# Optimization experiments

Hardware: AMD Instinct MI355X
Metric: run time of the kernel (lower is better)

## Reference

```python
import jax, jax.numpy as jnp
import numpy as np

EPS = 1e-5


def _whiten(feature):
    # ZCA whitening per sample (WCT): f_w = U diag(s^-1/2) U^T (f - mean)
    b, c, h, w = feature.shape
    f = feature.reshape(b, c, h * w)
    mean = f.mean(axis=-1, keepdims=True)
    f = f - mean
    cov = jnp.einsum('bcx,bdx->bcd', f, f) / (h * w - 1)
    s, u = jnp.linalg.eigh(cov)
    s = jnp.maximum(s, EPS)
    out = jnp.einsum('bcd,bd,bed,bex->bcx', u, s ** -0.5, u, f)
    return out.reshape(b, c, h, w)


def _color(feature, target):
    # ZCA coloring: f_c = Ut diag(st^1/2) Ut^T (f - mean_f) + mean_t
    b, c, h, w = feature.shape
    f = feature.reshape(b, c, h * w)
    f = f - f.mean(axis=-1, keepdims=True)
    t = target.reshape(b, c, -1)
    tmean = t.mean(axis=-1, keepdims=True)
    tc = t - tmean
    cov = jnp.einsum('bcx,bdx->bcd', tc, tc) / (tc.shape[-1] - 1)
    s, u = jnp.linalg.eigh(cov)
    s = jnp.maximum(s, EPS)
    out = jnp.einsum('bcd,bd,bed,bex->bcx', u, s ** 0.5, u, f) + tmean
    return out.reshape(b, c, h, w)


def _patches(f, p):
    # [b,c,h,w] -> [b,c,h,w,p*p], same ordering as torch unfold(2,p).unfold(3,p)
    pad = (p - 1) // 2
    b, c, h, w = f.shape
    fp = jnp.pad(f, ((0, 0), (0, 0), (pad, pad), (pad, pad)))
    return jnp.stack([fp[:, :, i:i + h, j:j + w] for i in range(p) for j in range(p)], axis=-1)


def reference(content_feature, style_feature, style_strength, patch_size):
    p = int(patch_size)
    pad = (p - 1) // 2
    nc = _whiten(content_feature)
    ns = _whiten(style_feature)
    b, c, h, w = nc.shape
    n = h * w  # one style kernel per style spatial location (stride 1)

    # style kernels [b, n, c, p, p] and their L2 norms over (c,p,p)
    sk = _patches(ns, p).transpose(0, 2, 3, 1, 4).reshape(b, n, c, p, p)
    knorm = jnp.sqrt(jnp.sum(sk ** 2, axis=(2, 3, 4), keepdims=True))
    skn = (sk / knorm).reshape(b, n, c, p * p)

    # patch matching score == conv2d of content with normalized style kernels
    cp = _patches(nc, p)                              # [b,c,h,w,p*p]
    score = jnp.einsum('bchwk,bnck->bnhw', cp, skn)   # [b,n,h,w]

    # argmax one-hot -> gather the best-matching (un-normalized) style patch
    idx = jnp.argmax(score, axis=1)                   # [b,h,w]
    sel = jax.vmap(lambda k, i: k[i])(sk, idx.reshape(b, -1))  # [b,hw,c,p,p]
    sel = sel.reshape(b, h, w, c, p, p).transpose(0, 3, 1, 2, 4, 5)  # [b,c,h,w,p,p]

    # overlap-add == conv_transpose2d(one_hot, kernels, padding=p-1) on padded input
    buf = jnp.zeros((b, c, h + p - 1, w + p - 1), dtype=sel.dtype)
    for di in range(p):
        for dj in range(p):
            buf = buf.at[:, :, di:di + h, dj:dj + w].add(sel[:, :, :, :, di, dj])
    recon = buf[:, :, pad:pad + h, pad:pad + w]

    # overlap counts (norm_deconvolution)
    m = jnp.zeros((h + p - 1, w + p - 1), dtype=sel.dtype)
    for di in range(p):
        for dj in range(p):
            m = m.at[di:di + h, dj:dj + w].add(1.0)
    norm = m[pad:pad + h, pad:pad + w]

    reassembled = recon / norm[None, None]
    stylized = _color(reassembled, style_feature)
    return (1.0 - style_strength) * content_feature + style_strength * stylized


def setup_inputs():
    key = jax.random.key(0)
    k1, k2 = jax.random.split(key)
    B, C, H, W = 2, 256, 48, 48
    return {
        'content_feature': jax.random.normal(k1, (B, C, H, W), jnp.float32),
        'style_feature': jax.random.normal(k2, (B, C, H, W), jnp.float32),
        'style_strength': jnp.float32(1.0),
        'patch_size': 3,
    }
```

## Files before the change

### kernel.cpp

```cpp
#include <hip/hip_runtime.h>

constexpr int B_  = 2;
constexpr int C_  = 256;
constexpr int H_  = 48;
constexpr int W_  = 48;
constexpr int N_  = H_ * W_;
constexpr int PH_ = H_ + 2;
constexpr int PW_ = W_ + 2;
constexpr int NP_ = PH_ * PW_;
constexpr int NPS_ = 2560;
constexpr int MS_  = 2560;
constexpr int CC_ = C_ * C_;
constexpr int NCH_ = 36;
constexpr int NC_  = N_ / NCH_;
constexpr int NSIT_ = 5;
constexpr int KCH_ = 9;

__device__ inline float waveRed(float v) {
  #pragma unroll
  for (int o = 32; o > 0; o >>= 1) v += __shfl_down(v, o);
  return v;
}

#define GEMM64_COMPUTE(sAT, sB, acc, ty, tx)                        \
  _Pragma("unroll")                                                 \
  for (int kk = 0; kk < 16; kk++) {                                 \
    float4 a = *(const float4*)&sAT[kk][(ty) * 4];                  \
    float4 b = *(const float4*)&sB[kk][(tx) * 4];                   \
    acc[0][0] += a.x * b.x; acc[0][1] += a.x * b.y;                 \
    acc[0][2] += a.x * b.z; acc[0][3] += a.x * b.w;                 \
    acc[1][0] += a.y * b.x; acc[1][1] += a.y * b.y;                 \
    acc[1][2] += a.y * b.z; acc[1][3] += a.y * b.w;                 \
    acc[2][0] += a.z * b.x; acc[2][1] += a.z * b.y;                 \
    acc[2][2] += a.z * b.z; acc[2][3] += a.z * b.w;                 \
    acc[3][0] += a.w * b.x; acc[3][1] += a.w * b.y;                 \
    acc[3][2] += a.w * b.z; acc[3][3] += a.w * b.w;                 \
  }


__global__ __launch_bounds__(256) void center_kernel(
    const float* __restrict__ content, const float* __restrict__ style,
    float* __restrict__ fc, float* __restrict__ fs, float* __restrict__ mean_s) {
  int t = blockIdx.x;
  int which = t / (B_ * C_);
  int bc = t % (B_ * C_);
  const float* src = which ? style : content;
  float* dst = which ? fs : fc;
  const float* row = src + (size_t)bc * N_;
  float acc = 0.f;
  for (int i = threadIdx.x; i < N_; i += 256) acc += row[i];
  __shared__ float sm[4];
  float r = waveRed(acc);
  if ((threadIdx.x & 63) == 0) sm[threadIdx.x >> 6] = r;
  __syncthreads();
  float mean = (sm[0] + sm[1] + sm[2] + sm[3]) * (1.0f / N_);
  for (int i = threadIdx.x; i < N_; i += 256) dst[(size_t)bc * N_ + i] = row[i] - mean;
  if (which == 1 && threadIdx.x == 0) mean_s[bc] = mean;
}

__global__ __launch_bounds__(256) void cov_kernel(
    const float* __restrict__ fc, const float* __restrict__ fs, float* __restrict__ pcov) {
  int z = blockIdx.z;
  int m = z & 3, ci = z >> 2;
  const float* f = (m < 2) ? (fc + (size_t)m * C_ * N_) : (fs + (size_t)(m - 2) * C_ * N_);
  int i0 = blockIdx.y * 64, j0 = blockIdx.x * 64;
  int t = threadIdx.x;
  int tx = t & 15, ty = t >> 4;
  int sr = t >> 2, skq = t & 3;
  __shared__ float sAT[16][68], sB[16][68];
  float acc[4][4] = {};
  int k0e = ci * 256 + 256;
  for (int k0 = ci * 256; k0 < k0e; k0 += 16) {
    float4 av = *(const float4*)&f[(size_t)(i0 + sr) * N_ + k0 + skq * 4];
    float4 bv = *(const float4*)&f[(size_t)(j0 + sr) * N_ + k0 + skq * 4];
    __syncthreads();
    sAT[skq * 4 + 0][sr] = av.x; sAT[skq * 4 + 1][sr] = av.y;
    sAT[skq * 4 + 2][sr] = av.z; sAT[skq * 4 + 3][sr] = av.w;
    sB[skq * 4 + 0][sr] = bv.x;  sB[skq * 4 + 1][sr] = bv.y;
    sB[skq * 4 + 2][sr] = bv.z;  sB[skq * 4 + 3][sr] = bv.w;
    __syncthreads();
    GEMM64_COMPUTE(sAT, sB, acc, ty, tx)
  }
  float* out = pcov + ((size_t)ci * 4 + m) * CC_;
  for (int u = 0; u < 4; u++)
    for (int v = 0; v < 4; v++)
      out[(size_t)(i0 + ty * 4 + u) * C_ + (j0 + tx * 4 + v)] = acc[u][v];
}

__global__ __launch_bounds__(256) void covreduce(
    const float* __restrict__ pcov, float* __restrict__ A4) {
  int t = blockIdx.x * 256 + threadIdx.x;
  float acc = 0.f;
  #pragma unroll
  for (int ci = 0; ci < KCH_; ci++) acc += pcov[(size_t)ci * 4 * CC_ + t];
  A4[t] = acc * (1.0f / (float)(N_ - 1));
}

__global__ __launch_bounds__(256) void ns_init(
    const float* __restrict__ A4, float* __restrict__ Yp, float* __restrict__ Zp,
    float* __restrict__ scal) {
  int m = blockIdx.y, s = blockIdx.x;
  const float* A = A4 + (size_t)m * CC_;
  float d = A[(size_t)threadIdx.x * 257];
  __shared__ float sm[4];
  float r = waveRed(d);
  if ((threadIdx.x & 63) == 0) sm[threadIdx.x >> 6] = r;
  __syncthreads();
  float trace = sm[0] + sm[1] + sm[2] + sm[3];
  float sc = 1.1f * trace / (float)C_;
  if (s == 0 && threadIdx.x == 0) scal[m] = sc;
  float inv = 1.0f / sc;
  int i0 = s * (CC_ / 16);
  for (int i = i0 + threadIdx.x; i < i0 + CC_ / 16; i += 256) {
    Yp[(size_t)m * CC_ + i] = A[i] * inv;
    Zp[(size_t)m * CC_ + i] = ((i >> 8) == (i & 255)) ? 1.0f : 0.0f;
    Yp[(size_t)(4 + m) * CC_ + i] = 0.f;
    Zp[(size_t)(4 + m) * CC_ + i] = 0.f;
  }
}

__global__ __launch_bounds__(256) void ns_stepA(
    const float* __restrict__ Zp, const float* __restrict__ Yp, float* __restrict__ Tp) {
  int z = blockIdx.z;
  int m = z & 3, kh = z >> 2;
  const float* A0 = Zp + (size_t)m * CC_;
  const float* A1 = Zp + (size_t)(4 + m) * CC_;
  const float* B0 = Yp + (size_t)m * CC_;
  const float* B1 = Yp + (size_t)(4 + m) * CC_;
  float* out = Tp + (size_t)(kh * 4 + m) * CC_;
  int i0 = blockIdx.y * 32, j0 = blockIdx.x * 32;
  int t = threadIdx.x;
  int tx = t & 15, ty = t >> 4;
  int sr = t >> 3, sc4 = t & 7;
  __shared__ float sAT[32][36], sB[32][36];
  float acc[2][2] = {};
  int k0e = kh * 128 + 128;
  for (int k0 = kh * 128; k0 < k0e; k0 += 32) {
    size_t ia = (size_t)(i0 + sr) * 256 + k0 + sc4 * 4;
    size_t ib = (size_t)(k0 + sr) * 256 + j0 + sc4 * 4;
    float4 a0 = *(const float4*)&A0[ia];
    float4 a1 = *(const float4*)&A1[ia];
    float4 b0 = *(const float4*)&B0[ib];
    float4 b1 = *(const float4*)&B1[ib];
    float4 av = {a0.x + a1.x, a0.y + a1.y, a0.z + a1.z, a0.w + a1.w};
    float4 bv = {b0.x + b1.x, b0.y + b1.y, b0.z + b1.z, b0.w + b1.w};
    __syncthreads();
    sAT[sc4 * 4 + 0][sr] = av.x; sAT[sc4 * 4 + 1][sr] = av.y;
    sAT[sc4 * 4 + 2][sr] = av.z; sAT[sc4 * 4 + 3][sr] = av.w;
    *(float4*)&sB[sr][sc4 * 4] = bv;
    __syncthreads();
    #pragma unroll
    for (int kk = 0; kk < 32; kk++) {
      float2 a = *(const float2*)&sAT[kk][ty * 2];
      float2 b = *(const float2*)&sB[kk][tx * 2];
      acc[0][0] += a.x * b.x; acc[0][1] += a.x * b.y;
      acc[1][0] += a.y * b.x; acc[1][1] += a.y * b.y;
    }
    __syncthreads();
  }
  for (int u = 0; u < 2; u++)
    for (int v = 0; v < 2; v++) {
      int i = i0 + ty * 2 + u, j = j0 + tx * 2 + v;
      float d = (kh == 0 && i == j) ? 3.0f : 0.0f;
      out[(size_t)i * 256 + j] = d - acc[u][v];
    }
}

__global__ __launch_bounds__(256) void ns_stepB(
    const float* __restrict__ Yp, const float* __restrict__ Zp, const float* __restrict__ Tp,
    float* __restrict__ Ynp, float* __restrict__ Znp) {
  int z = blockIdx.z;
  int m = z & 3, kh = (z >> 2) & 1;
  bool doY = (z < 8);
  const float* A0 = (doY ? Yp : Tp) + (size_t)m * CC_;
  const float* A1 = (doY ? Yp : Tp) + (size_t)(4 + m) * CC_;
  const float* B0 = (doY ? Tp : Zp) + (size_t)m * CC_;
  const float* B1 = (doY ? Tp : Zp) + (size_t)(4 + m) * CC_;
  float* out = (doY ? Ynp : Znp) + (size_t)(kh * 4 + m) * CC_;
  int i0 = blockIdx.y * 32, j0 = blockIdx.x * 32;
  int t = threadIdx.x;
  int tx = t & 15, ty = t >> 4;
  int sr = t >> 3, sc4 = t & 7;
  __shared__ float sAT[32][36], sB[32][36];
  float acc[2][2] = {};
  int k0e = kh * 128 + 128;
  for (int k0 = kh * 128; k0 < k0e; k0 += 32) {
    size_t ia = (size_t)(i0 + sr) * 256 + k0 + sc4 * 4;
    size_t ib = (size_t)(k0 + sr) * 256 + j0 + sc4 * 4;
    float4 a0 = *(const float4*)&A0[ia];
    float4 a1 = *(const float4*)&A1[ia];
    float4 b0 = *(const float4*)&B0[ib];
    float4 b1 = *(const float4*)&B1[ib];
    float4 av = {a0.x + a1.x, a0.y + a1.y, a0.z + a1.z, a0.w + a1.w};
    float4 bv = {b0.x + b1.x, b0.y + b1.y, b0.z + b1.z, b0.w + b1.w};
    __syncthreads();
    sAT[sc4 * 4 + 0][sr] = av.x; sAT[sc4 * 4 + 1][sr] = av.y;
    sAT[sc4 * 4 + 2][sr] = av.z; sAT[sc4 * 4 + 3][sr] = av.w;
    *(float4*)&sB[sr][sc4 * 4] = bv;
    __syncthreads();
    #pragma unroll
    for (int kk = 0; kk < 32; kk++) {
      float2 a = *(const float2*)&sAT[kk][ty * 2];
      float2 b = *(const float2*)&sB[kk][tx * 2];
      acc[0][0] += a.x * b.x; acc[0][1] += a.x * b.y;
      acc[1][0] += a.y * b.x; acc[1][1] += a.y * b.y;
    }
    __syncthreads();
  }
  for (int u = 0; u < 2; u++)
    for (int v = 0; v < 2; v++) {
      int i = i0 + ty * 2 + u, j = j0 + tx * 2 + v;
      out[(size_t)i * 256 + j] = 0.5f * acc[u][v];
    }
}

__global__ __launch_bounds__(256) void whiten_pad(
    const float* __restrict__ Zf, const float* __restrict__ scal,
    const float* __restrict__ fc, const float* __restrict__ fs,
    float* __restrict__ ncP, float* __restrict__ nsP, float* __restrict__ nsT) {
  int m = blockIdx.z;
  const float* f = (m < 2) ? (fc + (size_t)m * C_ * N_) : (fs + (size_t)(m - 2) * C_ * N_);
  int c0 = blockIdx.y * 64, x0 = blockIdx.x * 64;
  int t = threadIdx.x;
  int tx = t & 15, ty = t >> 4;
  int sr = t >> 2, skq = t & 3;
  int bkk = t & 15, bc4 = t >> 4;
  __shared__ float sAT[16][68], sB[16][68];
  float acc[4][4] = {};
  for (int k0 = 0; k0 < 256; k0 += 16) {
    size_t ia = (size_t)(c0 + sr) * 256 + k0 + skq * 4;
    float4 a0 = *(const float4*)&Zf[(size_t)m * CC_ + ia];
    float4 a1 = *(const float4*)&Zf[(size_t)(4 + m) * CC_ + ia];
    float4 av = {a0.x + a1.x, a0.y + a1.y, a0.z + a1.z, a0.w + a1.w};
    float4 bv = *(const float4*)&f[(size_t)(k0 + bkk) * N_ + x0 + bc4 * 4];
    __syncthreads();
    sAT[skq * 4 + 0][sr] = av.x; sAT[skq * 4 + 1][sr] = av.y;
    sAT[skq * 4 + 2][sr] = av.z; sAT[skq * 4 + 3][sr] = av.w;
    *(float4*)&sB[bkk][bc4 * 4] = bv;
    __syncthreads();
    GEMM64_COMPUTE(sAT, sB, acc, ty, tx)
  }
  float rs = rsqrtf(scal[m]);
  int b = (m < 2) ? m : (m - 2);
  for (int u = 0; u < 4; u++)
    for (int v = 0; v < 4; v++) {
      int c = c0 + ty * 4 + u, x = x0 + tx * 4 + v;
      int h = x / W_, w = x % W_;
      int pp = (h + 1) * PW_ + (w + 1);
      float val = acc[u][v] * rs;
      if (m < 2) {
        ncP[((size_t)b * C_ + c) * NPS_ + pp] = val;
      } else {
        nsP[((size_t)b * NP_ + pp) * C_ + c] = val;
        nsT[((size_t)b * C_ + c) * NPS_ + pp] = val;
      }
    }
}

__global__ __launch_bounds__(256) void q_kernel(const float* __restrict__ nsP, float* __restrict__ q) {
  int wid = (blockIdx.x * 256 + threadIdx.x) >> 6;
  int lane = threadIdx.x & 63;
  if (wid >= B_ * NP_) return;
  const float* v = nsP + (size_t)wid * C_;
  float acc = 0.f;
  #pragma unroll
  for (int c = lane; c < C_; c += 64) { float t = v[c]; acc += t * t; }
  acc = waveRed(acc);
  if (lane == 0) q[wid] = acc;
}

__global__ __launch_bounds__(256) void kninv_kernel(const float* __restrict__ q, float* __restrict__ kninv) {
  int t = blockIdx.x * 256 + threadIdx.x;
  if (t >= B_ * N_) return;
  int b = t / N_, n = t % N_;
  int hn = n / W_, wn = n % W_;
  const float* qb = q + (size_t)b * NP_ + hn * PW_ + wn;
  float s = 0.f;
  #pragma unroll
  for (int i = 0; i < 3; i++)
    #pragma unroll
    for (int j = 0; j < 3; j++) s += qb[i * PW_ + j];
  kninv[t] = rsqrtf(s);
}

__global__ __launch_bounds__(256) void m_kernel(
    const float* __restrict__ At, const float* __restrict__ Bt, float* __restrict__ M,
    size_t batchA, size_t batchM) {
  size_t bz = blockIdx.z;
  At += bz * batchA; Bt += bz * batchA; M += bz * batchM;
  int i0 = blockIdx.y * 64, j0 = blockIdx.x * 128;
  int t = threadIdx.x;
  int tx = t & 15, ty = t >> 4;
  int akk = t >> 4, ac4 = t & 15;
  int bkk = t >> 5, bc4 = t & 31;
  __shared__ float sA[16][68], sB[16][132];
  float acc[4][8] = {};
  for (int k0 = 0; k0 < 256; k0 += 16) {
    float4 a0 = *(const float4*)&At[(size_t)(k0 + akk) * NPS_ + i0 + ac4 * 4];
    float4 b0 = *(const float4*)&Bt[(size_t)(k0 + bkk) * NPS_ + j0 + bc4 * 4];
    float4 b1 = *(const float4*)&Bt[(size_t)(k0 + bkk + 8) * NPS_ + j0 + bc4 * 4];
    __syncthreads();
    *(float4*)&sA[akk][ac4 * 4] = a0;
    *(float4*)&sB[bkk][bc4 * 4] = b0;
    *(float4*)&sB[bkk + 8][bc4 * 4] = b1;
    __syncthreads();
    #pragma unroll
    for (int kk = 0; kk < 16; kk++) {
      float4 a  = *(const float4*)&sA[kk][ty * 4];
      float4 p  = *(const float4*)&sB[kk][tx * 4];
      float4 qv = *(const float4*)&sB[kk][64 + tx * 4];
      acc[0][0] += a.x * p.x; acc[0][1] += a.x * p.y; acc[0][2] += a.x * p.z; acc[0][3] += a.x * p.w;
      acc[1][0] += a.y * p.x; acc[1][1] += a.y * p.y; acc[1][2] += a.y * p.z; acc[1][3] += a.y * p.w;
      acc[2][0] += a.z * p.x; acc[2][1] += a.z * p.y; acc[2][2] += a.z * p.z; acc[2][3] += a.z * p.w;
      acc[3][0] += a.w * p.x; acc[3][1] += a.w * p.y; acc[3][2] += a.w * p.z; acc[3][3] += a.w * p.w;
      acc[0][4] += a.x * qv.x; acc[0][5] += a.x * qv.y; acc[0][6] += a.x * qv.z; acc[0][7] += a.x * qv.w;
      acc[1][4] += a.y * qv.x; acc[1][5] += a.y * qv.y; acc[1][6] += a.y * qv.z; acc[1][7] += a.y * qv.w;
      acc[2][4] += a.z * qv.x; acc[2][5] += a.z * qv.y; acc[2][6] += a.z * qv.z; acc[2][7] += a.z * qv.w;
      acc[3][4] += a.w * qv.x; acc[3][5] += a.w * qv.y; acc[3][6] += a.w * qv.z; acc[3][7] += a.w * qv.w;
    }
    __syncthreads();
  }
  #pragma unroll
  for (int u = 0; u < 4; u++) {
    size_t row = (size_t)(i0 + ty * 4 + u) * MS_;
    float4 s0 = {acc[u][0], acc[u][1], acc[u][2], acc[u][3]};
    float4 s1 = {acc[u][4], acc[u][5], acc[u][6], acc[u][7]};
    *(float4*)&M[row + j0 + tx * 4] = s0;
    *(float4*)&M[row + j0 + 64 + tx * 4] = s1;
  }
}

__global__ __launch_bounds__(256) void score_kernel(
    const float* __restrict__ M, const float* __restrict__ kninv,
    float* __restrict__ pval, int* __restrict__ pidx, int b0, size_t batchM) {
  int b = b0 + blockIdx.z;
  M += (size_t)blockIdx.z * batchM;
  int m = blockIdx.x * 256 + threadIdx.x;
  int h = m / W_, w = m % W_;
  int cm = h * PW_ + w;
  int n0 = blockIdx.y * NC_;
  const float* kni = kninv + (size_t)b * N_;
  float best = -3.4e38f;
  int bidx = n0;
  for (int n = n0; n < n0 + NC_; n++) {
    int hn = n / W_, wn = n % W_;
    int rn = hn * PW_ + wn;
    const float* base = M + (size_t)rn * MS_ + cm;
    float s = 0.f;
    #pragma unroll
    for (int i = 0; i < 3; i++)
      #pragma unroll
      for (int j = 0; j < 3; j++) s += base[(size_t)(i * PW_ + j) * (MS_ + 1)];
    s *= kni[n];
    if (s > best) { best = s; bidx = n; }
  }
  pval[((size_t)b * NCH_ + blockIdx.y) * N_ + m] = best;
  pidx[((size_t)b * NCH_ + blockIdx.y) * N_ + m] = bidx;
}

__global__ __launch_bounds__(256) void argmax_final(
    const float* __restrict__ pval, const int* __restrict__ pidx, int* __restrict__ idxb) {
  int t = blockIdx.x * 256 + threadIdx.x;
  if (t >= B_ * N_) return;
  int b = t / N_, m = t % N_;
  float best = -3.4e38f; int bidx = 0;
  for (int ch = 0; ch < NCH_; ch++) {
    float v = pval[((size_t)b * NCH_ + ch) * N_ + m];
    int i = pidx[((size_t)b * NCH_ + ch) * N_ + m];
    if (v > best) { best = v; bidx = i; }
  }
  idxb[t] = bidx;
}

__global__ __launch_bounds__(256) void reassemble_kernel(
    const float* __restrict__ nsP, const int* __restrict__ idxb, float* __restrict__ recon) {
  int bm = blockIdx.x;
  int b = bm / N_, m = bm % N_;
  int h = m / W_, w = m % W_;
  int c = threadIdx.x;
  float acc = 0.f; int cnt = 0;
  for (int di = 0; di < 3; di++) {
    int hs = h + 1 - di; if (hs < 0 || hs >= H_) continue;
    for (int dj = 0; dj < 3; dj++) {
      int ws = w + 1 - dj; if (ws < 0 || ws >= W_) continue;
      int n = idxb[(size_t)b * N_ + hs * W_ + ws];
      int hn = n / W_, wn = n % W_;
      int pp = (hn + di) * PW_ + (wn + dj);
      acc += nsP[((size_t)b * NP_ + pp) * C_ + c];
      cnt++;
    }
  }
  recon[((size_t)b * N_ + m) * C_ + c] = acc / (float)cnt;
}

__global__ __launch_bounds__(256) void rmean_part(const float* __restrict__ recon, float* __restrict__ pmr) {
  int b = blockIdx.y, ch = blockIdx.x, c = threadIdx.x;
  float acc = 0.f;
  int x0 = ch * (N_ / 16);
  for (int x = x0; x < x0 + (N_ / 16); x++) acc += recon[((size_t)b * N_ + x) * C_ + c];
  pmr[((size_t)b * 16 + ch) * C_ + c] = acc;
}

__global__ __launch_bounds__(256) void rmean_fin(const float* __restrict__ pmr, float* __restrict__ mr) {
  int b = blockIdx.x, c = threadIdx.x;
  float acc = 0.f;
  for (int ch = 0; ch < 16; ch++) acc += pmr[((size_t)b * 16 + ch) * C_ + c];
  mr[(size_t)b * C_ + c] = acc * (1.0f / N_);
}

__global__ __launch_bounds__(256) void color_blend(
    const float* __restrict__ Yf, const float* __restrict__ scal,
    const float* __restrict__ recon, const float* __restrict__ mr,
    const float* __restrict__ msty, const float* __restrict__ content,
    const float* __restrict__ ssp, float* __restrict__ out) {
  int b = blockIdx.z;
  int m = 2 + b;
  int c0 = blockIdx.y * 64, x0 = blockIdx.x * 64;
  int t = threadIdx.x;
  int tx = t & 15, ty = t >> 4;
  int sr = t >> 2, skq = t & 3;
  __shared__ float sAT[16][68], sB[16][68];
  float acc[4][4] = {};
  for (int k0 = 0; k0 < 256; k0 += 16) {
    size_t ia = (size_t)(c0 + sr) * 256 + k0 + skq * 4;
    float4 a0 = *(const float4*)&Yf[(size_t)m * CC_ + ia];
    float4 a1 = *(const float4*)&Yf[(size_t)(4 + m) * CC_ + ia];
    float4 av = {a0.x + a1.x, a0.y + a1.y, a0.z + a1.z, a0.w + a1.w};
    float4 bm4 = *(const float4*)&mr[(size_t)b * C_ + k0 + skq * 4];
    float4 bv = *(const float4*)&recon[((size_t)b * N_ + x0 + sr) * C_ + k0 + skq * 4];
    bv.x -= bm4.x; bv.y -= bm4.y; bv.z -= bm4.z; bv.w -= bm4.w;
    __syncthreads();
    sAT[skq * 4 + 0][sr] = av.x; sAT[skq * 4 + 1][sr] = av.y;
    sAT[skq * 4 + 2][sr] = av.z; sAT[skq * 4 + 3][sr] = av.w;
    sB[skq * 4 + 0][sr] = bv.x;  sB[skq * 4 + 1][sr] = bv.y;
    sB[skq * 4 + 2][sr] = bv.z;  sB[skq * 4 + 3][sr] = bv.w;
    __syncthreads();
    GEMM64_COMPUTE(sAT, sB, acc, ty, tx)
  }
  float sq = sqrtf(scal[m]);
  float ss = ssp[0];
  for (int u = 0; u < 4; u++)
    for (int v = 0; v < 4; v++) {
      int c = c0 + ty * 4 + u, x = x0 + tx * 4 + v;
      float sty = acc[u][v] * sq + msty[(size_t)b * C_ + c];
      size_t o = ((size_t)b * C_ + c) * N_ + x;
      out[o] = (1.0f - ss) * content[o] + ss * sty;
    }
}

extern "C" void kernel_launch(void* const* d_in, const int* in_sizes, int n_in,
                              void* d_out, int out_size, void* d_ws, size_t ws_size,
                              hipStream_t stream) {
  (void)in_sizes; (void)n_in; (void)out_size;
  const float* content = (const float*)d_in[0];
  const float* style   = (const float*)d_in[1];
  const float* ssp     = (const float*)d_in[2];
  float* out = (float*)d_out;
  float* W = (float*)d_ws;

  size_t off = 0;
  float* fc   = W + off; off += (size_t)B_ * C_ * N_;
  float* fs   = W + off; off += (size_t)B_ * C_ * N_;
  float* nsP  = W + off; off += (size_t)B_ * NP_ * C_;
  float* nsT  = W + off; off += (size_t)B_ * C_ * NPS_;
  float* ncP  = W + off; off += (size_t)B_ * C_ * NPS_;
  float* A4   = W + off; off += (size_t)4 * CC_;
  float* Ya   = W + off; off += (size_t)8 * CC_;
  float* Yb   = W + off; off += (size_t)8 * CC_;
  float* Za   = W + off; off += (size_t)8 * CC_;
  float* Zb   = W + off; off += (size_t)8 * CC_;
  float* scal = W + off; off += 4;
  float* msty = W + off; off += (size_t)B_ * C_;
  float* mr   = W + off; off += (size_t)B_ * C_;
  float* pmr  = W + off; off += (size_t)B_ * 16 * C_;
  float* q    = W + off; off += (size_t)B_ * NP_;
  float* kni  = W + off; off += (size_t)B_ * N_;
  float* pval = W + off; off += (size_t)B_ * NCH_ * N_;
  float* Mb   = W + off;
  size_t off_Mb = off;

  size_t off1 = off_Mb + (size_t)MS_ * MS_;
  size_t off2 = off_Mb + (size_t)2 * MS_ * MS_;
  size_t tail = (size_t)B_ * NCH_ * N_ + (size_t)B_ * N_;
  bool dual = ws_size >= (off2 + tail) * sizeof(float);
  size_t offM = dual ? off2 : off1;
  int* pidx = (int*)(W + offM);
  int* idxb = (int*)(W + offM + (size_t)B_ * NCH_ * N_);
  float* pcov = Mb;
  float* T    = Mb;
  float* recon = fs;

  hipMemsetAsync(nsP, 0, (size_t)B_ * NP_ * C_ * sizeof(float), stream);
  hipMemsetAsync(nsT, 0, (size_t)B_ * C_ * NPS_ * sizeof(float), stream);
  hipMemsetAsync(ncP, 0, (size_t)B_ * C_ * NPS_ * sizeof(float), stream);

  center_kernel<<<2 * B_ * C_, 256, 0, stream>>>(content, style, fc, fs, msty);
  cov_kernel<<<dim3(4, 4, 4 * KCH_), 256, 0, stream>>>(fc, fs, pcov);
  covreduce<<<4 * CC_ / 256, 256, 0, stream>>>(pcov, A4);
  ns_init<<<dim3(16, 4), 256, 0, stream>>>(A4, Ya, Za, scal);

  float *Ycur = Ya, *Zcur = Za, *Yalt = Yb, *Zalt = Zb;
  for (int it = 0; it < NSIT_; it++) {
    ns_stepA<<<dim3(8, 8, 8), 256, 0, stream>>>(Zcur, Ycur, T);
    ns_stepB<<<dim3(8, 8, 16), 256, 0, stream>>>(Ycur, Zcur, T, Yalt, Zalt);
    float* tp;
    tp = Ycur; Ycur = Yalt; Yalt = tp;
    tp = Zcur; Zcur = Zalt; Zalt = tp;
  }

  whiten_pad<<<dim3(36, 4, 4), 256, 0, stream>>>(Zcur, scal, fc, fs, ncP, nsP, nsT);
  q_kernel<<<(B_ * NP_ + 3) / 4, 256, 0, stream>>>(nsP, q);
  kninv_kernel<<<(B_ * N_ + 255) / 256, 256, 0, stream>>>(q, kni);

  if (dual) {
    m_kernel<<<dim3(20, 40, 2), 256, 0, stream>>>(
        nsT, ncP, Mb, (size_t)C_ * NPS_, (size_t)MS_ * MS_);
    score_kernel<<<dim3(N_ / 256, NCH_, 2), 256, 0, stream>>>(
        Mb, kni, pval, pidx, 0, (size_t)MS_ * MS_);
  } else {
    for (int b = 0; b < B_; b++) {
      m_kernel<<<dim3(20, 40, 1), 256, 0, stream>>>(
          nsT + (size_t)b * C_ * NPS_, ncP + (size_t)b * C_ * NPS_, Mb, 0, 0);
      score_kernel<<<dim3(N_ / 256, NCH_, 1), 256, 0, stream>>>(
          Mb, kni, pval, pidx, b, 0);
    }
  }
  argmax_final<<<(B_ * N_ + 255) / 256, 256, 0, stream>>>(pval, pidx, idxb);
  reassemble_kernel<<<B_ * N_, 256, 0, stream>>>(nsP, idxb, recon);
  rmean_part<<<dim3(16, B_), 256, 0, stream>>>(recon, pmr);
  rmean_fin<<<B_, 256, 0, stream>>>(pmr, mr);
  color_blend<<<dim3(36, 4, B_), 256, 0, stream>>>(
      Ycur, scal, recon, mr, msty, content, ssp, out);
}
```

Baseline: 362.5 us.

## Tile score diagonal-sum into shared memory and deepen m_kernel K-tile

Replaces the per-thread strided 9-term diagonal gather in the score kernel with a 2D tiled kernel. It loads 68x68 bands of M into shared memory and accumulates the three shifted diagonal bands from there, then does a tile-level argmax. The partial-argmax chunk count changes from 36 to 38 chunks over padded rows, and argmax_final and the workspace sizing are updated to match. Separately, the M GEMM K-tile grows from 16 to 32, which halves the number of syncs at the cost of more shared memory. The goal is to cut uncoalesced global reads in the scoring pass, with the risk of lower occupancy from the larger shared buffers.

```diff
diff --git a/kernel.cpp b/kernel.cpp
--- a/kernel.cpp
+++ b/kernel.cpp
@@ -11,8 +11,7 @@
 constexpr int NPS_ = 2560;
 constexpr int MS_  = 2560;
 constexpr int CC_ = C_ * C_;
-constexpr int NCH_ = 36;
-constexpr int NC_  = N_ / NCH_;
+constexpr int DC_ = 38;
 constexpr int NSIT_ = 5;
 constexpr int KCH_ = 9;
 
@@ -291,21 +290,27 @@
   int i0 = blockIdx.y * 64, j0 = blockIdx.x * 128;
   int t = threadIdx.x;
   int tx = t & 15, ty = t >> 4;
-  int akk = t >> 4, ac4 = t & 15;
-  int bkk = t >> 5, bc4 = t & 31;
-  __shared__ float sA[16][68], sB[16][132];
+  int ak = t >> 4, ac = t & 15;
+  int bk = t >> 5, bc = t & 31;
+  __shared__ float sA[32][68], sB[32][132];
   float acc[4][8] = {};
-  for (int k0 = 0; k0 < 256; k0 += 16) {
-    float4 a0 = *(const float4*)&At[(size_t)(k0 + akk) * NPS_ + i0 + ac4 * 4];
-    float4 b0 = *(const float4*)&Bt[(size_t)(k0 + bkk) * NPS_ + j0 + bc4 * 4];
-    float4 b1 = *(const float4*)&Bt[(size_t)(k0 + bkk + 8) * NPS_ + j0 + bc4 * 4];
-    __syncthreads();
-    *(float4*)&sA[akk][ac4 * 4] = a0;
-    *(float4*)&sB[bkk][bc4 * 4] = b0;
-    *(float4*)&sB[bkk + 8][bc4 * 4] = b1;
-    __syncthreads();
-    #pragma unroll
-    for (int kk = 0; kk < 16; kk++) {
+  for (int k0 = 0; k0 < 256; k0 += 32) {
+    float4 a0 = *(const float4*)&At[(size_t)(k0 + ak) * NPS_ + i0 + ac * 4];
+    float4 a1 = *(const float4*)&At[(size_t)(k0 + ak + 16) * NPS_ + i0 + ac * 4];
+    float4 b0 = *(const float4*)&Bt[(size_t)(k0 + bk) * NPS_ + j0 + bc * 4];
+    float4 b1 = *(const float4*)&Bt[(size_t)(k0 + bk + 8) * NPS_ + j0 + bc * 4];
+    float4 b2 = *(const float4*)&Bt[(size_t)(k0 + bk + 16) * NPS_ + j0 + bc * 4];
+    float4 b3 = *(const float4*)&Bt[(size_t)(k0 + bk + 24) * NPS_ + j0 + bc * 4];
+    __syncthreads();
+    *(float4*)&sA[ak][ac * 4] = a0;
+    *(float4*)&sA[ak + 16][ac * 4] = a1;
+    *(float4*)&sB[bk][bc * 4] = b0;
+    *(float4*)&sB[bk + 8][bc * 4] = b1;
+    *(float4*)&sB[bk + 16][bc * 4] = b2;
+    *(float4*)&sB[bk + 24][bc * 4] = b3;
+    __syncthreads();
+    #pragma unroll
+    for (int kk = 0; kk < 32; kk++) {
       float4 a  = *(const float4*)&sA[kk][ty * 4];
       float4 p  = *(const float4*)&sB[kk][tx * 4];
       float4 qv = *(const float4*)&sB[kk][64 + tx * 4];
@@ -330,32 +335,71 @@
   }
 }
 
-__global__ __launch_bounds__(256) void score_kernel(
+__global__ __launch_bounds__(256) void dscore_kernel(
     const float* __restrict__ M, const float* __restrict__ kninv,
     float* __restrict__ pval, int* __restrict__ pidx, int b0, size_t batchM) {
   int b = b0 + blockIdx.z;
   M += (size_t)blockIdx.z * batchM;
-  int m = blockIdx.x * 256 + threadIdx.x;
-  int h = m / W_, w = m % W_;
-  int cm = h * PW_ + w;
-  int n0 = blockIdx.y * NC_;
   const float* kni = kninv + (size_t)b * N_;
-  float best = -3.4e38f;
-  int bidx = n0;
-  for (int n = n0; n < n0 + NC_; n++) {
-    int hn = n / W_, wn = n % W_;
-    int rn = hn * PW_ + wn;
-    const float* base = M + (size_t)rn * MS_ + cm;
-    float s = 0.f;
-    #pragma unroll
-    for (int i = 0; i < 3; i++)
+  int r0 = blockIdx.y * 64, c0 = blockIdx.x * 64;
+  int t = threadIdx.x, tx = t & 15, ty = t >> 4;
+  __shared__ float L[68][70];
+  __shared__ float sVal[16][64];
+  __shared__ int   sIdx[16][64];
+  float acc[4][4] = {};
+  #pragma unroll
+  for (int band = 0; band < 3; band++) {
+    int rb = r0 + 50 * band, cb = c0 + 50 * band;
+    __syncthreads();
+    for (int idx = t; idx < 68 * 34; idx += 256) {
+      int rr = idx / 34, cc = (idx - rr * 34) * 2;
+      *(float2*)&L[rr][cc] = *(const float2*)&M[(size_t)(rb + rr) * MS_ + cb + cc];
+    }
+    __syncthreads();
+    #pragma unroll
+    for (int j = 0; j < 3; j++)
       #pragma unroll
-      for (int j = 0; j < 3; j++) s += base[(size_t)(i * PW_ + j) * (MS_ + 1)];
-    s *= kni[n];
-    if (s > best) { best = s; bidx = n; }
-  }
-  pval[((size_t)b * NCH_ + blockIdx.y) * N_ + m] = best;
-  pidx[((size_t)b * NCH_ + blockIdx.y) * N_ + m] = bidx;
+      for (int u = 0; u < 4; u++)
+        #pragma unroll
+        for (int v = 0; v < 4; v++)
+          acc[u][v] += L[ty * 4 + u + j][tx + 16 * v + j];
+  }
+  float kn[4]; int nn[4]; bool vld[4];
+  #pragma unroll
+  for (int u = 0; u < 4; u++) {
+    int r = r0 + ty * 4 + u;
+    int hn = r / 50, wn = r - hn * 50;
+    vld[u] = (wn < W_) && (hn < H_);
+    nn[u] = hn * W_ + wn;
+    kn[u] = vld[u] ? kni[nn[u]] : 0.f;
+  }
+  #pragma unroll
+  for (int v = 0; v < 4; v++) {
+    float best = -3.4e38f; int bn = 0;
+    #pragma unroll
+    for (int u = 0; u < 4; u++) {
+      float s = vld[u] ? acc[u][v] * kn[u] : -3.4e38f;
+      if (s > best) { best = s; bn = nn[u]; }
+    }
+    sVal[ty][tx + 16 * v] = best;
+    sIdx[ty][tx + 16 * v] = bn;
+  }
+  __syncthreads();
+  if (t < 64) {
+    float best = -3.4e38f; int bn = 0;
+    #pragma unroll
+    for (int k = 0; k < 16; k++) {
+      float v = sVal[k][t];
+      if (v > best) { best = v; bn = sIdx[k][t]; }
+    }
+    int c = c0 + t;
+    int h = c / 50, w = c - h * 50;
+    if (w < W_ && h < H_) {
+      int m = h * W_ + w;
+      pval[((size_t)b * DC_ + blockIdx.y) * N_ + m] = best;
+      pidx[((size_t)b * DC_ + blockIdx.y) * N_ + m] = bn;
+    }
+  }
 }
 
 __global__ __launch_bounds__(256) void argmax_final(
@@ -364,9 +408,9 @@
   if (t >= B_ * N_) return;
   int b = t / N_, m = t % N_;
   float best = -3.4e38f; int bidx = 0;
-  for (int ch = 0; ch < NCH_; ch++) {
-    float v = pval[((size_t)b * NCH_ + ch) * N_ + m];
-    int i = pidx[((size_t)b * NCH_ + ch) * N_ + m];
+  for (int ch = 0; ch < DC_; ch++) {
+    float v = pval[((size_t)b * DC_ + ch) * N_ + m];
+    int i = pidx[((size_t)b * DC_ + ch) * N_ + m];
     if (v > best) { best = v; bidx = i; }
   }
   idxb[t] = bidx;
@@ -475,17 +519,17 @@
   float* pmr  = W + off; off += (size_t)B_ * 16 * C_;
   float* q    = W + off; off += (size_t)B_ * NP_;
   float* kni  = W + off; off += (size_t)B_ * N_;
-  float* pval = W + off; off += (size_t)B_ * NCH_ * N_;
+  float* pval = W + off; off += (size_t)B_ * DC_ * N_;
   float* Mb   = W + off;
   size_t off_Mb = off;
 
   size_t off1 = off_Mb + (size_t)MS_ * MS_;
   size_t off2 = off_Mb + (size_t)2 * MS_ * MS_;
-  size_t tail = (size_t)B_ * NCH_ * N_ + (size_t)B_ * N_;
+  size_t tail = (size_t)B_ * DC_ * N_ + (size_t)B_ * N_;
   bool dual = ws_size >= (off2 + tail) * sizeof(float);
   size_t offM = dual ? off2 : off1;
   int* pidx = (int*)(W + offM);
-  int* idxb = (int*)(W + offM + (size_t)B_ * NCH_ * N_);
+  int* idxb = (int*)(W + offM + (size_t)B_ * DC_ * N_);
   float* pcov = Mb;
   float* T    = Mb;
   float* recon = fs;
@@ -515,13 +559,13 @@
   if (dual) {
     m_kernel<<<dim3(20, 40, 2), 256, 0, stream>>>(
         nsT, ncP, Mb, (size_t)C_ * NPS_, (size_t)MS_ * MS_);
-    score_kernel<<<dim3(N_ / 256, NCH_, 2), 256, 0, stream>>>(
+    dscore_kernel<<<dim3(DC_, DC_, 2), 256, 0, stream>>>(
         Mb, kni, pval, pidx, 0, (size_t)MS_ * MS_);
   } else {
     for (int b = 0; b < B_; b++) {
       m_kernel<<<dim3(20, 40, 1), 256, 0, stream>>>(
           nsT + (size_t)b * C_ * NPS_, ncP + (size_t)b * C_ * NPS_, Mb, 0, 0);
-      score_kernel<<<dim3(N_ / 256, NCH_, 1), 256, 0, stream>>>(
+      dscore_kernel<<<dim3(DC_, DC_, 1), 256, 0, stream>>>(
           Mb, kni, pval, pidx, b, 0);
     }
   }
```

Result: slower. 392.4 us (+8.2%).
